# Performance work log

Hardware: AMD Instinct MI355X
Metric: run time of the kernel (lower is better)

Reference implementation:

```python
import jax, jax.numpy as jnp
import numpy as np
import math

SQRT32 = math.sqrt(32.0)


def _l2norm(x, eps=1e-12):
    # matches torch.nn.functional.normalize(dim=-1): x / max(||x||, eps)
    n = jnp.linalg.norm(x, axis=-1, keepdims=True)
    return x / jnp.maximum(n, eps)


def setup_inputs() -> dict:
    key = jax.random.key(0)
    k1, k2 = jax.random.split(key)
    z = jax.random.normal(k1, (8, 256, 32, 32), dtype=jnp.float32)
    # trunc_normal_(std=0.02) init approximated by scaled normal
    embed_weight = jax.random.normal(k2, (16384, 256), dtype=jnp.float32) * 0.02
    return {"z": z, "embed_weight": embed_weight}


def reference(z, embed_weight):
    # z: [b, d, h, w] channel-first -> pack to [b*h*w, d]
    b, d, h, w = z.shape
    zf = jnp.transpose(z, (0, 2, 3, 1)).reshape(-1, d)  # [N, d]

    # l2_norm=True, no predefined codebook: distance = -z @ normalize(E)^T
    ew = _l2norm(embed_weight)                          # [K, d]
    dist = -(zf @ ew.T)                                 # [N, K]
    min_encoding_indices = jnp.argmin(dist, axis=1)     # [N]

    # gather UNnormalized embedding rows, then normalize (as in source)
    z_q = _l2norm(embed_weight[min_encoding_indices])   # [N, d]

    # straight-through estimator
    z_q = zf + jax.lax.stop_gradient(z_q - zf)

    loss = jnp.zeros((1,), dtype=z.dtype)

    # unpack to [b, h, w, d]
    zq_bhwd = z_q.reshape(b, h, w, d)
    # torch .long() truncates toward zero; astype(int) does the same
    bit_indices = (zq_bhwd * SQRT32).astype(jnp.int32) + 4
    zq_out = jnp.transpose(zq_bhwd, (0, 3, 1, 2))       # [b, d, h, w]

    return zq_out, min_encoding_indices, bit_indices, loss
```

## Files before the change

kernel.cpp:

```cpp
#include <hip/hip_runtime.h>
#include <math.h>

#define D      256
#define K      16384
#define NPTS   8192
#define DELTA  0.2f
#define LCAP   1024
#define MAXCAP 4000000u

#define O_IDX  2097152
#define O_BIT  2105344
#define O_LOSS 4202496

typedef __attribute__((ext_vector_type(8))) short bf16x8;
typedef __attribute__((ext_vector_type(4))) float f32x4;
typedef unsigned long long u64;

__device__ __forceinline__ unsigned f2s(float f) {
    unsigned u = __float_as_uint(f);
    return (u & 0x80000000u) ? ~u : (u | 0x80000000u);
}
__device__ __forceinline__ float s2f(unsigned s) {
    return __uint_as_float((s & 0x80000000u) ? (s & 0x7fffffffu) : ~s);
}
__device__ __forceinline__ unsigned short f2bf(float f) {
    unsigned u = __float_as_uint(f);
    u += 0x7fffu + ((u >> 16) & 1u);
    return (unsigned short)(u >> 16);
}


__global__ __launch_bounds__(256) void prep(const float* __restrict__ E,
                                            const float* __restrict__ z,
                                            float* __restrict__ den,
                                            unsigned short* __restrict__ ewbT,
                                            unsigned short* __restrict__ zfbT,
                                            float* __restrict__ zf32,
                                            unsigned* __restrict__ gmax,
                                            u64* __restrict__ keys,
                                            unsigned* __restrict__ cnt) {
    const int blk = blockIdx.x, tid = threadIdx.x;
    if (blk < 512) {
        const int lane = tid & 63, wave = tid >> 6;
        if (blk < 32)        gmax[blk * 256 + tid] = 0u;
        else if (blk < 64)   keys[(blk - 32) * 256 + tid] = 0ull;
        else if (blk == 64 && tid < 2) cnt[tid] = 0u;
        #pragma unroll
        for (int j = 0; j < 8; ++j) {
            const int row = blk * 32 + wave * 8 + j;
            const float4 v = *(const float4*)(E + (size_t)row * D + lane * 4);
            float ss = v.x * v.x + v.y * v.y + v.z * v.z + v.w * v.w;
            #pragma unroll
            for (int o = 1; o < 64; o <<= 1) ss += __shfl_xor(ss, o);
            const float dn = fmaxf(sqrtf(ss), 1e-12f);
            const unsigned lo = (unsigned)f2bf(v.x / dn) | ((unsigned)f2bf(v.y / dn) << 16);
            const unsigned hi = (unsigned)f2bf(v.z / dn) | ((unsigned)f2bf(v.w / dn) << 16);
            *(uint2*)(ewbT + ((size_t)(lane >> 1) * K + row) * 8 + (lane & 1) * 4)
                = make_uint2(lo, hi);
            if (lane == 0) den[row] = dn;
        }
    } else {
        const int bi = blk - 512;
        const int b = bi >> 4, hw0 = (bi & 15) * 64;
        __shared__ float t[64][65];
        for (int dc = 0; dc < D; dc += 64) {
            #pragma unroll
            for (int it = 0; it < 16; ++it) {
                const int idx = it * 256 + tid;
                const int dl = idx >> 6, hw = idx & 63;
                t[dl][hw] = z[(size_t)(b * 256 + dc + dl) * 1024 + hw0 + hw];
            }
            __syncthreads();
            #pragma unroll
            for (int it = 0; it < 16; ++it) {
                const int idx = it * 256 + tid;
                const int pl = idx >> 6, dl = idx & 63;
                const float v = t[dl][pl];
                const int p = b * 1024 + hw0 + pl, k = dc + dl;
                zfbT[((size_t)(k >> 3) * NPTS + p) * 8 + (k & 7)] = f2bf(v);
                zf32[(size_t)p * D + k] = v;
            }
            __syncthreads();
        }
    }
}

#define GEMM_CORE()                                                                 \
    f32x4 acc[4][4];                                                                \
    _Pragma("unroll")                                                               \
    for (int i = 0; i < 4; ++i)                                                     \
        _Pragma("unroll")                                                           \
        for (int j = 0; j < 4; ++j) acc[i][j] = (f32x4){0.f, 0.f, 0.f, 0.f};        \
    {                                                                               \
        const unsigned short* pA = zfbT + ((size_t)quad * NPTS + m0 + wm * 64 + col) * 8; \
        const unsigned short* pB = ewbT + ((size_t)quad * K    + n0 + wn * 64 + col) * 8; \
        _Pragma("unroll")                                                           \
        for (int dc = 0; dc < 8; ++dc) {                                            \
            bf16x8 af[4], bfr[4];                                                   \
            _Pragma("unroll")                                                       \
            for (int mt = 0; mt < 4; ++mt)                                          \
                af[mt] = *(const bf16x8*)(pA + (size_t)dc * 4 * NPTS * 8 + mt * 128);\
            _Pragma("unroll")                                                       \
            for (int nt = 0; nt < 4; ++nt)                                          \
                bfr[nt] = *(const bf16x8*)(pB + (size_t)dc * 4 * K * 8 + nt * 128); \
            _Pragma("unroll")                                                       \
            for (int mt = 0; mt < 4; ++mt)                                          \
                _Pragma("unroll")                                                   \
                for (int nt = 0; nt < 4; ++nt)                                      \
                    acc[mt][nt] = __builtin_amdgcn_mfma_f32_16x16x32_bf16(af[mt], bfr[nt], \
                                                                          acc[mt][nt], 0, 0, 0); \
        }                                                                           \
    }

__global__ __launch_bounds__(256, 3) void score_seed(const unsigned short* __restrict__ zfbT,
                                                     const unsigned short* __restrict__ ewbT,
                                                     unsigned* __restrict__ gmax,
                                                     u64* __restrict__ cand,
                                                     unsigned* __restrict__ cnt,
                                                     unsigned cap) {
    __shared__ unsigned thrS[128];
    __shared__ u64 lbuf[LCAP];
    __shared__ unsigned lcount, lbase;

    const int tid = threadIdx.x, lane = tid & 63, wave = tid >> 6;
    const int quad = lane >> 4, col = lane & 15;
    const int wm = wave >> 1, wn = wave & 1;
    const int m0 = blockIdx.x * 128;
    const int n0 = blockIdx.y * 128;
    const int shsrc = lane & 48;

    if (tid < 128) thrS[tid] = 0u;
    if (tid == 0) lcount = 0u;

    GEMM_CORE()
    __syncthreads();

    float red[4][4];
    #pragma unroll
    for (int mt = 0; mt < 4; ++mt)
        #pragma unroll
        for (int r = 0; r < 4; ++r)
            red[mt][r] = fmaxf(fmaxf(acc[mt][0][r], acc[mt][1][r]),
                               fmaxf(acc[mt][2][r], acc[mt][3][r]));
    #pragma unroll
    for (int off = 1; off < 16; off <<= 1)
        #pragma unroll
        for (int mt = 0; mt < 4; ++mt)
            #pragma unroll
            for (int r = 0; r < 4; ++r)
                red[mt][r] = fmaxf(red[mt][r], __shfl_xor(red[mt][r], off));
    #pragma unroll
    for (int mt = 0; mt < 4; ++mt)
        #pragma unroll
        for (int r = 0; r < 4; ++r) {
            const int pl = wm * 64 + mt * 16 + quad * 4 + r;
            unsigned cur = 0;
            if (col == 0) {
                const unsigned enc = f2s(red[mt][r]);
                const unsigned old = atomicMax(&thrS[pl], enc);
                cur = old > enc ? old : enc;
            }
            cur = (unsigned)__shfl((int)cur, shsrc);
            red[mt][r] = s2f(cur) - DELTA;
        }

    const int ncode0 = n0 + wn * 64 + col;
    #pragma unroll
    for (int mt = 0; mt < 4; ++mt) {
        #pragma unroll
        for (int r = 0; r < 4; ++r) {
            const float tp = red[mt][r];
            const unsigned pt = m0 + wm * 64 + mt * 16 + quad * 4 + r;
            #pragma unroll
            for (int nt = 0; nt < 4; ++nt) {
                const float v = acc[mt][nt][r];
                if (v >= tp) {
                    const unsigned slot = atomicAdd(&lcount, 1u);
                    const u64 e = ((u64)((pt << 14) | (unsigned)(ncode0 + nt * 16)) << 32)
                                  | f2s(v);
                    if (slot < LCAP) lbuf[slot] = e;
                    else {
                        const unsigned g = atomicAdd(cnt, 1u);
                        if (g < cap) cand[g] = e;
                    }
                }
            }
        }
    }

    __syncthreads();
    if (tid < 128) atomicMax(&gmax[m0 + tid], thrS[tid]);
    const unsigned m_ = lcount < LCAP ? lcount : LCAP;
    if (tid == 0) lbase = atomicAdd(cnt, m_);
    __syncthreads();
    for (unsigned i = tid; i < m_; i += 256) {
        const unsigned g = lbase + i;
        if (g < cap) cand[g] = lbuf[i];
    }
}

__global__ __launch_bounds__(256, 3) void score_main(const unsigned short* __restrict__ zfbT,
                                                     const unsigned short* __restrict__ ewbT,
                                                     const unsigned* __restrict__ gmax,
                                                     u64* __restrict__ cand,
                                                     unsigned* __restrict__ cnt,
                                                     unsigned cap) {
    __shared__ float thrL[128];
    __shared__ u64 lbuf[LCAP];
    __shared__ unsigned lcount, lbase;

    const int tid = threadIdx.x, lane = tid & 63, wave = tid >> 6;
    const int quad = lane >> 4, col = lane & 15;
    const int wm = wave >> 1, wn = wave & 1;
    const int m0 = blockIdx.x * 128;
    const int n0 = (16 + blockIdx.y) * 128;

    if (tid < 128) thrL[tid] = s2f(gmax[m0 + tid]) - DELTA;
    if (tid == 0) lcount = 0u;

    GEMM_CORE()
    __syncthreads();

    const int ncode0 = n0 + wn * 64 + col;
    #pragma unroll
    for (int mt = 0; mt < 4; ++mt) {
        #pragma unroll
        for (int r = 0; r < 4; ++r) {
            const int pl = wm * 64 + mt * 16 + quad * 4 + r;
            const float tp = thrL[pl];
            #pragma unroll
            for (int nt = 0; nt < 4; ++nt) {
                const float v = acc[mt][nt][r];
                if (v >= tp) {
                    const unsigned slot = atomicAdd(&lcount, 1u);
                    const u64 e = ((u64)(((unsigned)pl + m0) << 14 | (unsigned)(ncode0 + nt * 16)) << 32)
                                  | f2s(v);
                    if (slot < LCAP) lbuf[slot] = e;
                    else {
                        const unsigned g = atomicAdd(cnt, 1u);
                        if (g < cap) cand[g] = e;
                    }
                }
            }
        }
    }

    __syncthreads();
    const unsigned m_ = lcount < LCAP ? lcount : LCAP;
    if (tid == 0) lbase = atomicAdd(cnt, m_);
    __syncthreads();
    for (unsigned i = tid; i < m_; i += 256) {
        const unsigned g = lbase + i;
        if (g < cap) cand[g] = lbuf[i];
    }
}

__global__ __launch_bounds__(256) void cand_max(const u64* __restrict__ cand,
                                                const unsigned* __restrict__ cnt,
                                                unsigned* __restrict__ gmax,
                                                unsigned cap) {
    const unsigned total = min(cnt[0], cap);
    const unsigned stride = gridDim.x * 256;
    for (unsigned i = blockIdx.x * 256 + threadIdx.x; i < total; i += stride) {
        const u64 e = cand[i];
        atomicMax(&gmax[(unsigned)(e >> 46)], (unsigned)(e & 0xffffffffull));
    }
}

__global__ __launch_bounds__(256) void rescore(const float* __restrict__ zf32,
                                               const float* __restrict__ E,
                                               const float* __restrict__ den,
                                               const unsigned* __restrict__ gmax,
                                               const u64* __restrict__ cand,
                                               const unsigned* __restrict__ cnt,
                                               u64* __restrict__ keys,
                                               unsigned cap) {
    const unsigned total = min(cnt[0], cap);
    const int lane = threadIdx.x & 63;
    const unsigned w = (blockIdx.x * 256 + threadIdx.x) >> 6;
    const unsigned nw = gridDim.x * 4;
    for (unsigned base = w * 64; base < total; base += nw * 64) {
        const unsigned i = base + lane;
        u64 e = 0;
        bool keep = false;
        if (i < total) {
            e = cand[i];
            const int p = (int)(e >> 46);
            keep = (s2f((unsigned)(e & 0xffffffffull)) >= s2f(gmax[p]) - DELTA);
        }
        u64 mask = __ballot(keep);
        while (mask) {
            const int src = __ffsll((long long)mask) - 1;
            mask &= mask - 1;
            const unsigned pc = (unsigned)__shfl((int)(unsigned)(e >> 32), src);
            const int p = pc >> 14, c = pc & 16383;
            const float dinv = 1.0f / den[c];
            const float4 a = *(const float4*)(zf32 + (size_t)p * D + lane * 4);
            const float4 b = *(const float4*)(E + (size_t)c * D + lane * 4);
            float sv = fmaf(a.x, b.x * dinv, fmaf(a.y, b.y * dinv,
                       fmaf(a.z, b.z * dinv, a.w * (b.w * dinv))));
            #pragma unroll
            for (int o = 1; o < 64; o <<= 1) sv += __shfl_xor(sv, o);
            if (lane == 0)
                atomicMax(keys + p, ((u64)f2s(sv) << 32) | (unsigned)(16383 - c));
        }
    }
}

__global__ __launch_bounds__(256) void finalize(const float* __restrict__ E,
                                                const float* __restrict__ den,
                                                const u64* __restrict__ keys,
                                                float* __restrict__ out) {
    __shared__ float t[32][257];
    __shared__ int sIdx[32];
    __shared__ float sDen[32];
    const int tid = threadIdx.x;
    const int n0 = blockIdx.x * 32;
    if (tid < 32) {
        const u64 key = keys[n0 + tid];
        const int idx = 16383 - (int)(unsigned)(key & 0xffffffffull);
        sIdx[tid] = idx;
        sDen[tid] = den[idx];
        out[O_IDX + n0 + tid] = (float)idx;
    }
    __syncthreads();
    const float S = 5.65685424949238019520675489683895f;
    #pragma unroll 4
    for (int i = 0; i < 32; ++i) {
        const float v = E[(size_t)sIdx[i] * D + tid] / sDen[i];
        t[i][tid] = v;
        out[O_BIT + (size_t)(n0 + i) * D + tid] = (float)((int)(v * S) + 4);
    }
    __syncthreads();
    const int b = n0 >> 10, hw0 = n0 & 1023;
    const int hwl = tid & 31, cg = tid >> 5;
    #pragma unroll 4
    for (int cc = 0; cc < 32; ++cc) {
        const int c = cc * 8 + cg;
        out[(size_t)(b * 256 + c) * 1024 + hw0 + hwl] = t[hwl][c];
    }
    if (n0 == 0 && tid == 0) out[O_LOSS] = 0.0f;
}

extern "C" void kernel_launch(void* const* d_in, const int* in_sizes, int n_in,
                              void* d_out, int out_size, void* d_ws, size_t ws_size,
                              hipStream_t stream) {
    const float* z = (const float*)d_in[0];
    const float* E = (const float*)d_in[1];
    float* out = (float*)d_out;

    char* w = (char*)d_ws;
    unsigned short* ewbT = (unsigned short*)w;  w += (size_t)K * D * 2;
    unsigned short* zfbT = (unsigned short*)w;  w += (size_t)NPTS * D * 2;
    float*          zf32 = (float*)w;           w += (size_t)NPTS * D * 4;
    u64*            keys = (u64*)w;             w += (size_t)NPTS * 8;
    float*          den  = (float*)w;           w += (size_t)K * 4;
    unsigned*       gmax = (unsigned*)w;        w += (size_t)NPTS * 4;
    unsigned*       cnt  = (unsigned*)w;        w += 256;
    u64*            cand = (u64*)w;
    const size_t fixed = (size_t)(w - (char*)d_ws);
    const size_t avail = ws_size > fixed ? (ws_size - fixed) / 8 : 0;
    const unsigned cap = (unsigned)(avail < (size_t)MAXCAP ? avail : (size_t)MAXCAP);

    prep<<<640, 256, 0, stream>>>(E, z, den, ewbT, zfbT, zf32, gmax, keys, cnt);

    dim3 gpre(NPTS / 128, 16);
    score_seed<<<gpre, 256, 0, stream>>>(zfbT, ewbT, gmax, cand, cnt, cap);
    dim3 gmain(NPTS / 128, 112);
    score_main<<<gmain, 256, 0, stream>>>(zfbT, ewbT, gmax, cand, cnt, cap);

    cand_max<<<256, 256, 0, stream>>>(cand, cnt, gmax, cap);
    rescore<<<1024, 256, 0, stream>>>(zf32, E, den, gmax, cand, cnt, keys, cap);
    finalize<<<NPTS / 32, 256, 0, stream>>>(E, den, keys, out);
}
```

Before: 264.5 us.

## Stage GEMM operands through double-buffered LDS with async global-to-LDS loads

The GEMM core used to load A and B fragments straight from global memory into registers, so each wave issued duplicate loads with no overlap. It now copies each K-chunk into a double-buffered shared-memory tile using global_load_lds, with an XOR swizzle on row indices, and computes the MFMAs from LDS while the next chunk is in flight. This cuts redundant global traffic across waves and overlaps loads with compute. The cost is 32KB of LDS per block, which may limit occupancy at launch_bounds(256,3), plus extra barriers and a dependence on correct ordering of the async loads.

```diff
diff --git a/kernel.cpp b/kernel.cpp
--- a/kernel.cpp
+++ b/kernel.cpp
@@ -27,6 +27,12 @@
     unsigned u = __float_as_uint(f);
     u += 0x7fffu + ((u >> 16) & 1u);
     return (unsigned short)(u >> 16);
+}
+
+__device__ __forceinline__ void gload16(const unsigned short* g, unsigned short* l) {
+    __builtin_amdgcn_global_load_lds(
+        (const __attribute__((address_space(1))) unsigned int*)g,
+        (__attribute__((address_space(3))) unsigned int*)l, 16, 0, 0);
 }
 
 
@@ -85,32 +91,59 @@
     }
 }
 
+
+#define STAGE(buf, t)                                                               \
+    do {                                                                            \
+        const size_t oA_ = (size_t)(t) * (4 * NPTS * 8);                            \
+        const size_t oB_ = (size_t)(t) * (4 * K * 8);                               \
+        gload16(gA0_ + oA_, &sA[buf][tid * 8]);                                     \
+        gload16(gA1_ + oA_, &sA[buf][2048 + tid * 8]);                              \
+        gload16(gB0_ + oB_, &sB[buf][tid * 8]);                                     \
+        gload16(gB1_ + oB_, &sB[buf][2048 + tid * 8]);                              \
+    } while (0)
+
+#define COMPUTE(buf)                                                                \
+    do {                                                                            \
+        bf16x8 af_[4], bf_[4];                                                      \
+        const unsigned short* a_ = &sA[buf][(size_t)sbA_ * 8];                      \
+        const unsigned short* b_ = &sB[buf][(size_t)sbB_ * 8];                      \
+        _Pragma("unroll")                                                           \
+        for (int mt = 0; mt < 4; ++mt) {                                            \
+            af_[mt] = *(const bf16x8*)(a_ + mt * 128);                              \
+            bf_[mt] = *(const bf16x8*)(b_ + mt * 128);                              \
+        }                                                                           \
+        _Pragma("unroll")                                                           \
+        for (int mt = 0; mt < 4; ++mt)                                              \
+            _Pragma("unroll")                                                       \
+            for (int nt = 0; nt < 4; ++nt)                                          \
+                acc[mt][nt] = __builtin_amdgcn_mfma_f32_16x16x32_bf16(af_[mt], bf_[nt], \
+                                                                      acc[mt][nt], 0, 0, 0); \
+    } while (0)
+
 #define GEMM_CORE()                                                                 \
+    __shared__ unsigned short sA[2][4096];                                          \
+    __shared__ unsigned short sB[2][4096];                                          \
     f32x4 acc[4][4];                                                                \
     _Pragma("unroll")                                                               \
-    for (int i = 0; i < 4; ++i)                                                     \
+    for (int i_ = 0; i_ < 4; ++i_)                                                  \
         _Pragma("unroll")                                                           \
-        for (int j = 0; j < 4; ++j) acc[i][j] = (f32x4){0.f, 0.f, 0.f, 0.f};        \
-    {                                                                               \
-        const unsigned short* pA = zfbT + ((size_t)quad * NPTS + m0 + wm * 64 + col) * 8; \
-        const unsigned short* pB = ewbT + ((size_t)quad * K    + n0 + wn * 64 + col) * 8; \
-        _Pragma("unroll")                                                           \
-        for (int dc = 0; dc < 8; ++dc) {                                            \
-            bf16x8 af[4], bfr[4];                                                   \
-            _Pragma("unroll")                                                       \
-            for (int mt = 0; mt < 4; ++mt)                                          \
-                af[mt] = *(const bf16x8*)(pA + (size_t)dc * 4 * NPTS * 8 + mt * 128);\
-            _Pragma("unroll")                                                       \
-            for (int nt = 0; nt < 4; ++nt)                                          \
-                bfr[nt] = *(const bf16x8*)(pB + (size_t)dc * 4 * K * 8 + nt * 128); \
-            _Pragma("unroll")                                                       \
-            for (int mt = 0; mt < 4; ++mt)                                          \
-                _Pragma("unroll")                                                   \
-                for (int nt = 0; nt < 4; ++nt)                                      \
-                    acc[mt][nt] = __builtin_amdgcn_mfma_f32_16x16x32_bf16(af[mt], bfr[nt], \
-                                                                          acc[mt][nt], 0, 0, 0); \
-        }                                                                           \
-    }
+        for (int j_ = 0; j_ < 4; ++j_) acc[i_][j_] = (f32x4){0.f, 0.f, 0.f, 0.f};   \
+    const int q0_ = tid >> 7, q1_ = q0_ + 2, pp_ = tid & 127;                       \
+    const unsigned short* gA0_ = zfbT + ((size_t)q0_ * NPTS + m0 + (pp_ ^ (q0_ << 1))) * 8; \
+    const unsigned short* gA1_ = zfbT + ((size_t)q1_ * NPTS + m0 + (pp_ ^ (q1_ << 1))) * 8; \
+    const unsigned short* gB0_ = ewbT + ((size_t)q0_ * K + n0 + (pp_ ^ (q0_ << 1))) * 8; \
+    const unsigned short* gB1_ = ewbT + ((size_t)q1_ * K + n0 + (pp_ ^ (q1_ << 1))) * 8; \
+    const int sbA_ = quad * 128 + ((wm * 64 + col) ^ (quad << 1));                  \
+    const int sbB_ = quad * 128 + ((wn * 64 + col) ^ (quad << 1));                  \
+    STAGE(0, 0);                                                                    \
+    __syncthreads();                                                                \
+    _Pragma("unroll")                                                               \
+    for (int t_ = 0; t_ < 7; ++t_) {                                                \
+        STAGE((t_ & 1) ^ 1, t_ + 1);                                                \
+        COMPUTE(t_ & 1);                                                            \
+        __syncthreads();                                                            \
+    }                                                                               \
+    COMPUTE(1);
 
 __global__ __launch_bounds__(256, 3) void score_seed(const unsigned short* __restrict__ zfbT,
                                                      const unsigned short* __restrict__ ewbT,
```

Measured after the change: 261.6 us. No clear change (-1.1%).
